# Performance work log

Measured on AMD Instinct MI355X. Metric: run time of the kernel, lower is better.

Reference implementation:

```python
import jax, jax.numpy as jnp
import numpy as np

ALPHA = 0.2  # LeakyReLU negative slope (self.alpha)
NEG_INF = -1e9


def setup_inputs() -> dict:
    key = jax.random.key(0)
    k1, k2, k3, k4, k5 = jax.random.split(key, 5)
    N, Fin, Fout = 8192, 256, 128
    return {
        "input": jax.random.normal(k1, (N, Fin), dtype=jnp.float32),
        "W": jax.random.normal(k2, (Fin, Fout), dtype=jnp.float32) * 0.1,
        "c1": jax.random.normal(k3, (Fout, 1), dtype=jnp.float32) * 0.1,
        "c2": jax.random.normal(k4, (Fout, 1), dtype=jnp.float32) * 0.1,
        "adj": jax.random.randint(k5, (N, N), 0, 2, dtype=jnp.int32),
        "M": N,
    }


def reference(input, W, c1, c2, adj, M):
    # h: [N, Fout]
    h = input @ W
    # valid neighbor j for row x: adj[x, j] > 0 and h[j].sum() != 0
    valid = (adj[:M] > 0) & (jnp.sum(h, axis=1) != 0.0)[None, :]  # [M, N]
    # e[x, j] = leakyrelu(h[x] @ c1 + h[j] @ c2)
    s_dst = (h[:M] @ c1)            # [M, 1]
    s_src = (h @ c2).T              # [1, N]
    e = jax.nn.leaky_relu(s_dst + s_src, negative_slope=ALPHA)
    e = jnp.where(valid, e, NEG_INF)
    attn = jax.nn.softmax(e, axis=1)
    attn = jnp.where(valid, attn, 0.0)  # rows with no neighbors -> all-zero weights
    # dropout is identity at inference (training=False); pool=0 branch skipped
    h_prime = attn @ h              # [M, Fout]
    return jax.nn.elu(h_prime)
```

## Files before the change

kernel.cpp:

```cpp
#include <hip/hip_runtime.h>
#include <math.h>

typedef __attribute__((ext_vector_type(8))) short bf16x8;
typedef __attribute__((ext_vector_type(4))) float f32x4;

#define GAT_ALPHA 0.2f

static __device__ __forceinline__ unsigned short f2bf(float x) {
    unsigned u = __float_as_uint(x);
    u += 0x7fffu + ((u >> 16) & 1u);
    return (unsigned short)(u >> 16);
}
static __device__ __forceinline__ float bf2f(unsigned short b) {
    return __uint_as_float(((unsigned)b) << 16);
}

__global__ __launch_bounds__(512)
void k_prep(const float* __restrict__ input, const float* __restrict__ W,
            const float* __restrict__ c1, const float* __restrict__ c2,
            unsigned short* __restrict__ hb, float* __restrict__ ssx,
            float* __restrict__ sd, int N, int Fin, int Fout)
{
    __shared__ float in_lds[4][256];
    __shared__ float red[4][3];
    const int tid = threadIdx.x;
    const int r0 = blockIdx.x * 4;
    for (int idx = tid; idx < 4 * Fin; idx += 512) {
        int r = idx / Fin, c = idx - r * Fin;
        in_lds[r][c] = input[(size_t)(r0 + r) * Fin + c];
    }
    if (tid < 12) ((float*)red)[tid] = 0.f;
    __syncthreads();
    const int y = tid >> 7, f = tid & 127;
    float acc = 0.f;
    for (int k = 0; k < Fin; ++k)
        acc = fmaf(in_lds[y][k], W[(size_t)k * Fout + f], acc);
    const int row = r0 + y;
    hb[(size_t)row * Fout + f] = f2bf(acc);
    float rs = acc, sv = acc * c2[f], dv = acc * c1[f];
    for (int off = 32; off > 0; off >>= 1) {
        rs += __shfl_xor(rs, off);
        sv += __shfl_xor(sv, off);
        dv += __shfl_xor(dv, off);
    }
    if ((tid & 63) == 0) {
        atomicAdd(&red[y][0], rs);
        atomicAdd(&red[y][1], sv);
        atomicAdd(&red[y][2], dv);
    }
    __syncthreads();
    if (f == 0) {
        float rsum = red[y][0];
        ssx[row] = (rsum != 0.f) ? red[y][1] : -1e30f;
        sd[row]  = red[y][2];
    }
}

__global__ __launch_bounds__(1024)
void k_smax(const float* __restrict__ ssx, float* __restrict__ smax, int N)
{
    __shared__ float red[16];
    const int tid = threadIdx.x;
    float m = -3e38f;
    for (int i = tid; i < N; i += 1024) m = fmaxf(m, ssx[i]);
    for (int off = 32; off > 0; off >>= 1) m = fmaxf(m, __shfl_xor(m, off));
    if ((tid & 63) == 0) red[tid >> 6] = m;
    __syncthreads();
    if (tid == 0) {
        float mm = red[0];
        for (int i = 1; i < 16; ++i) mm = fmaxf(mm, red[i]);
        smax[0] = mm;
    }
}

__global__ __launch_bounds__(256)
void k_transpose(const unsigned short* __restrict__ hb, unsigned short* __restrict__ ht,
                 int N, int Fout)
{
    __shared__ unsigned short t[64][65];
    const int bx = blockIdx.x;
    const int by = blockIdx.y;
    const int tid = threadIdx.x;
    for (int i = 0; i < 16; ++i) {
        int idx = i * 256 + tid; int r = idx >> 6, c = idx & 63;
        t[r][c] = hb[(size_t)(bx * 64 + r) * Fout + by * 64 + c];
    }
    __syncthreads();
    for (int i = 0; i < 16; ++i) {
        int idx = i * 256 + tid; int r = idx >> 6, c = idx & 63;
        ht[(size_t)(by * 64 + r) * N + bx * 64 + c] = t[c][r];
    }
}

__global__ __launch_bounds__(512, 4)
void k_attn(const int* __restrict__ adj, const unsigned short* __restrict__ ht,
            const float* __restrict__ ssx, const float* __restrict__ sd,
            const float* __restrict__ smaxp, unsigned short* __restrict__ part,
            float* __restrict__ dpart, int N, int M, int chunk)
{
    extern __shared__ char smem[];
    unsigned* bits = (unsigned*)smem;
    char* btile = smem + 128 * (chunk >> 3);

    const int tid = threadIdx.x;
    const int rb  = blockIdx.x * 128;
    const int j0  = blockIdx.y * chunk;
    const int wpr = chunk >> 5;
    const int NT  = wpr;

    {
        const int gpr16 = chunk >> 4;
        const int gsh = 31 - __clz(gpr16);
        const int groups = 128 << gsh;
        unsigned short* bsh = (unsigned short*)smem;
        for (int g = tid; g < groups; g += 512) {
            const int rl = g >> gsh;
            const int jg = g & (gpr16 - 1);
            const int* ap = adj + (size_t)(rb + rl) * N + j0 + jg * 16;
            int4 v0 = *(const int4*)ap;
            int4 v1 = *(const int4*)(ap + 4);
            int4 v2 = *(const int4*)(ap + 8);
            int4 v3 = *(const int4*)(ap + 12);
            unsigned b = (unsigned)(v0.x > 0)         | ((unsigned)(v0.y > 0) << 1)
                       | ((unsigned)(v0.z > 0) << 2)  | ((unsigned)(v0.w > 0) << 3)
                       | ((unsigned)(v1.x > 0) << 4)  | ((unsigned)(v1.y > 0) << 5)
                       | ((unsigned)(v1.z > 0) << 6)  | ((unsigned)(v1.w > 0) << 7)
                       | ((unsigned)(v2.x > 0) << 8)  | ((unsigned)(v2.y > 0) << 9)
                       | ((unsigned)(v2.z > 0) << 10) | ((unsigned)(v2.w > 0) << 11)
                       | ((unsigned)(v3.x > 0) << 12) | ((unsigned)(v3.y > 0) << 13)
                       | ((unsigned)(v3.z > 0) << 14) | ((unsigned)(v3.w > 0) << 15);
            bsh[(rl * wpr + ((jg >> 1) ^ (rl & 7))) * 2 + (jg & 1)] = (unsigned short)b;
        }
    }

    const int w  = tid >> 6;
    const int l  = tid & 63;
    const int am = l & 15;
    const int kg = l >> 4;
    const int ams = am & 7;

    const int rl0 = w * 16 + am;
    const int r0 = rb + rl0;
    const float s0 = sd[r0];
    const float sm = smaxp[0];
    const float vb0 = s0 + sm;
    const float m0 = fmaxf(vb0, GAT_ALPHA * vb0);
    const int bw0 = rl0 * wpr;
    const float* __restrict__ sbase = ssx + j0 + 8 * kg;

    const int fw = tid >> 2, jp = tid & 3;
    const unsigned short* __restrict__ gstage = ht + (size_t)fw * N + j0 + jp * 8;
    const int cw = fw >> 4, amw = fw & 15;
    const int wslot = (((cw & 1) << 2) | jp) ^ (amw & 7);
    const int waddr = (fw >> 5) * 2048 + amw * 128 + wslot * 16;

    const int roffE = am * 128 + ((0 | kg) ^ ams) * 16;
    const int roffO = am * 128 + ((4 | kg) ^ ams) * 16;

    f32x4 acc[8];
    #pragma unroll
    for (int c = 0; c < 8; ++c) acc[c] = (f32x4){0.f, 0.f, 0.f, 0.f};
    float d0 = 0.f;

    __syncthreads();

    bf16x8 REG = *(const bf16x8*)gstage;
    float4 sC0 = *(const float4*)(sbase);
    float4 sC1 = *(const float4*)(sbase + 4);
    float4 sN0, sN1;

    auto PBUILD = [&](unsigned bw, const float4& u0, const float4& u1) -> bf16x8 {
        bf16x8 af;
        unsigned short* pu = (unsigned short*)&af;
        const float* f0 = (const float*)&u0;
        const float* f1 = (const float*)&u1;
        float d = 0.f;
        #pragma unroll
        for (int i = 0; i < 4; ++i) {
            float v = s0 + f0[i];
            float e = fminf(fmaxf(v, GAT_ALPHA * v) - m0, 0.f);
            float p = (bw & (1u << i)) ? __expf(e) : 0.f;
            pu[i] = f2bf(p); d += p;
        }
        #pragma unroll
        for (int i = 0; i < 4; ++i) {
            float v = s0 + f1[i];
            float e = fminf(fmaxf(v, GAT_ALPHA * v) - m0, 0.f);
            float p = (bw & (16u << i)) ? __expf(e) : 0.f;
            pu[4 + i] = f2bf(p); d += p;
        }
        d0 += d;
        return af;
    };

    auto STEP = [&](int jt, int par, float4& p0, float4& p1, float4& q0, float4& q1) {
        *(bf16x8*)(btile + par * 8192 + waddr) = REG;
        __syncthreads();
        const char* bt = btile + par * 8192;
        bf16x8 b0 = *(const bf16x8*)(bt + roffE);
        bf16x8 b1 = *(const bf16x8*)(bt + roffO);
        bf16x8 b2 = *(const bf16x8*)(bt + 2048 + roffE);
        bf16x8 b3 = *(const bf16x8*)(bt + 2048 + roffO);
        const unsigned bb = bits[bw0 + (jt ^ ams)] >> (8 * kg);
        const int nj = ((jt + 1 < NT) ? jt + 1 : 0) * 32;
        REG = *(const bf16x8*)(gstage + nj);
        q0 = *(const float4*)(sbase + nj);
        q1 = *(const float4*)(sbase + nj + 4);
        bf16x8 af = PBUILD(bb, p0, p1);
        acc[0] = __builtin_amdgcn_mfma_f32_16x16x32_bf16(af, b0, acc[0], 0, 0, 0);
        acc[1] = __builtin_amdgcn_mfma_f32_16x16x32_bf16(af, b1, acc[1], 0, 0, 0);
        acc[2] = __builtin_amdgcn_mfma_f32_16x16x32_bf16(af, b2, acc[2], 0, 0, 0);
        acc[3] = __builtin_amdgcn_mfma_f32_16x16x32_bf16(af, b3, acc[3], 0, 0, 0);
        bf16x8 b4 = *(const bf16x8*)(bt + 4096 + roffE);
        bf16x8 b5 = *(const bf16x8*)(bt + 4096 + roffO);
        bf16x8 b6 = *(const bf16x8*)(bt + 6144 + roffE);
        bf16x8 b7 = *(const bf16x8*)(bt + 6144 + roffO);
        acc[4] = __builtin_amdgcn_mfma_f32_16x16x32_bf16(af, b4, acc[4], 0, 0, 0);
        acc[5] = __builtin_amdgcn_mfma_f32_16x16x32_bf16(af, b5, acc[5], 0, 0, 0);
        acc[6] = __builtin_amdgcn_mfma_f32_16x16x32_bf16(af, b6, acc[6], 0, 0, 0);
        acc[7] = __builtin_amdgcn_mfma_f32_16x16x32_bf16(af, b7, acc[7], 0, 0, 0);
    };

    for (int jt = 0; jt + 1 < NT; jt += 2) {
        STEP(jt,     0, sC0, sC1, sN0, sN1);
        STEP(jt + 1, 1, sN0, sN1, sC0, sC1);
    }
    if (NT & 1) STEP(NT - 1, 0, sC0, sC1, sN0, sN1);

    d0 += __shfl_xor(d0, 16);
    d0 += __shfl_xor(d0, 32);
    if (kg == 0) dpart[(size_t)blockIdx.y * M + r0] = d0;

    unsigned short* pb = part + (size_t)blockIdx.y * M * 128
                       + ((((size_t)blockIdx.x * 8 + w) * 64 + l) * 32);
    #pragma unroll
    for (int ec = 0; ec < 4; ++ec) {
        const f32x4 x = acc[ec * 2];
        const f32x4 y = acc[ec * 2 + 1];
        bf16x8 pv;
        unsigned short* pp = (unsigned short*)&pv;
        pp[0] = f2bf(x[0]); pp[1] = f2bf(x[1]); pp[2] = f2bf(x[2]); pp[3] = f2bf(x[3]);
        pp[4] = f2bf(y[0]); pp[5] = f2bf(y[1]); pp[6] = f2bf(y[2]); pp[7] = f2bf(y[3]);
        *(bf16x8*)(pb + ec * 8) = pv;
    }
}

__global__ __launch_bounds__(256)
void k_dsum(const float* __restrict__ dpart, float* __restrict__ denom, int M, int NS)
{
    const int r = blockIdx.x * 256 + threadIdx.x;
    if (r < M) {
        float d = 0.f;
        for (int s = 0; s < NS; ++s) d += dpart[(size_t)s * M + r];
        denom[r] = d;
    }
}

__global__ __launch_bounds__(256)
void k_combine(const unsigned short* __restrict__ part, const float* __restrict__ denom,
               float* __restrict__ out, int M, int NS)
{
    const int idx = blockIdx.x * 256 + threadIdx.x;
    const int rbk = idx >> 11;
    const int rem = idx & 2047;
    const int w  = rem >> 8;
    const int l  = (rem >> 2) & 63;
    const int ec = rem & 3;
    const int am = l & 15, kg = l >> 4;

    float sums[8] = {0.f, 0.f, 0.f, 0.f, 0.f, 0.f, 0.f, 0.f};
    const unsigned short* p = part + (size_t)idx * 8;
    for (int s = 0; s < NS; ++s) {
        bf16x8 v = *(const bf16x8*)(p + (size_t)s * M * 128);
        const unsigned short* vp = (const unsigned short*)&v;
        #pragma unroll
        for (int i = 0; i < 8; ++i) sums[i] += bf2f(vp[i]);
    }
    const int rbase = rbk * 128 + w * 16 + kg * 4;
    #pragma unroll
    for (int reg = 0; reg < 4; ++reg) {
        const float dd = denom[rbase + reg];
        const float inv = (dd > 0.f) ? 1.f / dd : 0.f;
        #pragma unroll
        for (int half = 0; half < 2; ++half) {
            float x = sums[half * 4 + reg] * inv;
            x = (x > 0.f) ? x : expm1f(x);
            out[(size_t)(rbase + reg) * 128 + (ec * 2 + half) * 16 + am] = x;
        }
    }
}

extern "C" void kernel_launch(void* const* d_in, const int* in_sizes, int n_in,
                              void* d_out, int out_size, void* d_ws, size_t ws_size,
                              hipStream_t stream)
{
    const float* input = (const float*)d_in[0];
    const float* W     = (const float*)d_in[1];
    const float* c1    = (const float*)d_in[2];
    const float* c2    = (const float*)d_in[3];
    const int*   adj   = (const int*)d_in[4];

    const int Fout = in_sizes[2];
    const int Fin  = in_sizes[1] / Fout;
    const int N    = in_sizes[0] / Fin;
    const int M    = out_size / Fout;
    float* out = (float*)d_out;

    char* ws = (char*)d_ws;
    const size_t o_hb   = 0;
    const size_t o_ht   = o_hb + (size_t)N * Fout * 2;
    const size_t o_ssx  = o_ht + (size_t)N * Fout * 2;
    const size_t o_sd   = o_ssx + (size_t)N * 4;
    const size_t o_smax = o_sd + (size_t)N * 4;
    const size_t o_den  = o_smax + 64;
    const size_t o_dpart = o_den + (((size_t)M * 4 + 63) & ~63ULL);

    int NS = 16;
    size_t o_part = 0;
    while (NS >= 1) {
        size_t op = (o_dpart + (size_t)NS * M * 4 + 15) & ~15ULL;
        if (op + (size_t)NS * M * Fout * 2 <= ws_size) { o_part = op; break; }
        NS >>= 1;
    }
    const int chunk = N / NS;

    unsigned short* hb = (unsigned short*)(ws + o_hb);
    unsigned short* ht = (unsigned short*)(ws + o_ht);
    float* ssx   = (float*)(ws + o_ssx);
    float* sd    = (float*)(ws + o_sd);
    float* smax  = (float*)(ws + o_smax);
    float* denom = (float*)(ws + o_den);
    float* dpart = (float*)(ws + o_dpart);
    unsigned short* part = (unsigned short*)(ws + o_part);

    k_prep<<<N / 4, 512, 0, stream>>>(input, W, c1, c2, hb, ssx, sd, N, Fin, Fout);
    k_smax<<<1, 1024, 0, stream>>>(ssx, smax, N);
    k_transpose<<<dim3(N / 64, Fout / 64), 256, 0, stream>>>(hb, ht, N, Fout);

    const size_t smem_bytes = 128 * (size_t)(chunk >> 3) + 2 * 8192;
    k_attn<<<dim3(M / 128, NS), 512, smem_bytes, stream>>>(
        adj, ht, ssx, sd, smax, part, dpart, N, M, chunk);

    k_dsum<<<(M + 255) / 256, 256, 0, stream>>>(dpart, denom, M, NS);
    k_combine<<<M * Fout / 8 / 256, 256, 0, stream>>>(part, denom, out, M, NS);
}
```

Measured before the change: 160.0 us.

## Restructure attention kernel: direct adj register loads, 256-column LDS tiles, fixed NS=8

The attention kernel no longer packs adjacency into an LDS bitmask up front. Each lane now loads its adj ints directly from global memory, prefetched two k-steps ahead. The h^T tile is staged in 64KB LDS chunks of 256 columns with an XOR swizzle, and ssx values are cached in LDS, giving four barrier phases per block instead of one per 32 columns. The split count is fixed at 8 rather than chosen adaptively from workspace size. This cuts barriers and the bitmask prepass, but the fixed 64KB static LDS limits occupancy and exposes the stage loads without double buffering.

```diff
diff --git a/kernel.cpp b/kernel.cpp
--- a/kernel.cpp
+++ b/kernel.cpp
@@ -5,6 +5,7 @@
 typedef __attribute__((ext_vector_type(4))) float f32x4;
 
 #define GAT_ALPHA 0.2f
+#define NS 8
 
 static __device__ __forceinline__ unsigned short f2bf(float x) {
     unsigned u = __float_as_uint(x);
@@ -96,143 +97,102 @@
 void k_attn(const int* __restrict__ adj, const unsigned short* __restrict__ ht,
             const float* __restrict__ ssx, const float* __restrict__ sd,
             const float* __restrict__ smaxp, unsigned short* __restrict__ part,
-            float* __restrict__ dpart, int N, int M, int chunk)
-{
-    extern __shared__ char smem[];
-    unsigned* bits = (unsigned*)smem;
-    char* btile = smem + 128 * (chunk >> 3);
-
-    const int tid = threadIdx.x;
-    const int rb  = blockIdx.x * 128;
-    const int j0  = blockIdx.y * chunk;
-    const int wpr = chunk >> 5;
-    const int NT  = wpr;
-
-    {
-        const int gpr16 = chunk >> 4;
-        const int gsh = 31 - __clz(gpr16);
-        const int groups = 128 << gsh;
-        unsigned short* bsh = (unsigned short*)smem;
-        for (int g = tid; g < groups; g += 512) {
-            const int rl = g >> gsh;
-            const int jg = g & (gpr16 - 1);
-            const int* ap = adj + (size_t)(rb + rl) * N + j0 + jg * 16;
-            int4 v0 = *(const int4*)ap;
-            int4 v1 = *(const int4*)(ap + 4);
-            int4 v2 = *(const int4*)(ap + 8);
-            int4 v3 = *(const int4*)(ap + 12);
-            unsigned b = (unsigned)(v0.x > 0)         | ((unsigned)(v0.y > 0) << 1)
-                       | ((unsigned)(v0.z > 0) << 2)  | ((unsigned)(v0.w > 0) << 3)
-                       | ((unsigned)(v1.x > 0) << 4)  | ((unsigned)(v1.y > 0) << 5)
-                       | ((unsigned)(v1.z > 0) << 6)  | ((unsigned)(v1.w > 0) << 7)
-                       | ((unsigned)(v2.x > 0) << 8)  | ((unsigned)(v2.y > 0) << 9)
-                       | ((unsigned)(v2.z > 0) << 10) | ((unsigned)(v2.w > 0) << 11)
-                       | ((unsigned)(v3.x > 0) << 12) | ((unsigned)(v3.y > 0) << 13)
-                       | ((unsigned)(v3.z > 0) << 14) | ((unsigned)(v3.w > 0) << 15);
-            bsh[(rl * wpr + ((jg >> 1) ^ (rl & 7))) * 2 + (jg & 1)] = (unsigned short)b;
-        }
-    }
-
-    const int w  = tid >> 6;
-    const int l  = tid & 63;
-    const int am = l & 15;
-    const int kg = l >> 4;
-    const int ams = am & 7;
-
-    const int rl0 = w * 16 + am;
-    const int r0 = rb + rl0;
-    const float s0 = sd[r0];
+            float* __restrict__ dpart, int N, int M)
+{
+    __shared__ char btile[65536];
+    __shared__ float sxl[256];
+
+    const int tid = threadIdx.x;
+    const int w = tid >> 6, l = tid & 63, am = l & 15, kg = l >> 4, ams = am & 7;
+    const int bi = blockIdx.x, bj = blockIdx.y;
+    const int jch = N / NS;
+    const int j0 = bj * jch;
+    const int row = bi * 128 + w * 16 + am;
+
+    const float s0 = sd[row];
     const float sm = smaxp[0];
-    const float vb0 = s0 + sm;
-    const float m0 = fmaxf(vb0, GAT_ALPHA * vb0);
-    const int bw0 = rl0 * wpr;
-    const float* __restrict__ sbase = ssx + j0 + 8 * kg;
-
-    const int fw = tid >> 2, jp = tid & 3;
-    const unsigned short* __restrict__ gstage = ht + (size_t)fw * N + j0 + jp * 8;
-    const int cw = fw >> 4, amw = fw & 15;
-    const int wslot = (((cw & 1) << 2) | jp) ^ (amw & 7);
-    const int waddr = (fw >> 5) * 2048 + amw * 128 + wslot * 16;
-
-    const int roffE = am * 128 + ((0 | kg) ^ ams) * 16;
-    const int roffO = am * 128 + ((4 | kg) ^ ams) * 16;
+    const float vb = s0 + sm;
+    const float m0 = fmaxf(vb, GAT_ALPHA * vb);
+
+    const int fb  = tid >> 5;
+    const int pos = tid & 31;
+    const int rbl = am * 512;
+
+    const int* __restrict__ aptr = adj + (size_t)row * N + j0 + kg * 8;
 
     f32x4 acc[8];
     #pragma unroll
     for (int c = 0; c < 8; ++c) acc[c] = (f32x4){0.f, 0.f, 0.f, 0.f};
     float d0 = 0.f;
 
-    __syncthreads();
-
-    bf16x8 REG = *(const bf16x8*)gstage;
-    float4 sC0 = *(const float4*)(sbase);
-    float4 sC1 = *(const float4*)(sbase + 4);
-    float4 sN0, sN1;
-
-    auto PBUILD = [&](unsigned bw, const float4& u0, const float4& u1) -> bf16x8 {
+    int4 cA0 = *(const int4*)(aptr);
+    int4 cA1 = *(const int4*)(aptr + 4);
+    int4 cB0 = *(const int4*)(aptr + 32);
+    int4 cB1 = *(const int4*)(aptr + 36);
+
+    auto KS = [&](int q, int4& c0, int4& c1) {
+        const int ks = q & 7;
+        float4 x0 = *(const float4*)&sxl[ks * 32 + kg * 8];
+        float4 x1 = *(const float4*)&sxl[ks * 32 + kg * 8 + 4];
         bf16x8 af;
-        unsigned short* pu = (unsigned short*)&af;
-        const float* f0 = (const float*)&u0;
-        const float* f1 = (const float*)&u1;
-        float d = 0.f;
-        #pragma unroll
-        for (int i = 0; i < 4; ++i) {
-            float v = s0 + f0[i];
-            float e = fminf(fmaxf(v, GAT_ALPHA * v) - m0, 0.f);
-            float p = (bw & (1u << i)) ? __expf(e) : 0.f;
-            pu[i] = f2bf(p); d += p;
-        }
-        #pragma unroll
-        for (int i = 0; i < 4; ++i) {
-            float v = s0 + f1[i];
-            float e = fminf(fmaxf(v, GAT_ALPHA * v) - m0, 0.f);
-            float p = (bw & (16u << i)) ? __expf(e) : 0.f;
-            pu[4 + i] = f2bf(p); d += p;
-        }
-        d0 += d;
-        return af;
+        {
+            unsigned short* pu = (unsigned short*)&af;
+            const int* ai0 = (const int*)&c0;
+            const int* ai1 = (const int*)&c1;
+            const float* f0 = (const float*)&x0;
+            const float* f1 = (const float*)&x1;
+            float d = 0.f;
+            #pragma unroll
+            for (int i = 0; i < 4; ++i) {
+                float v = s0 + f0[i];
+                float e = fminf(fmaxf(v, GAT_ALPHA * v) - m0, 0.f);
+                float p = (ai0[i] > 0) ? __expf(e) : 0.f;
+                pu[i] = f2bf(p); d += p;
+            }
+            #pragma unroll
+            for (int i = 0; i < 4; ++i) {
+                float v = s0 + f1[i];
+                float e = fminf(fmaxf(v, GAT_ALPHA * v) - m0, 0.f);
+                float p = (ai1[i] > 0) ? __expf(e) : 0.f;
+                pu[4 + i] = f2bf(p); d += p;
+            }
+            d0 += d;
+        }
+        const int qq = (q + 2 < 4 * 8) ? q + 2 : 4 * 8 - 1;
+        c0 = *(const int4*)(aptr + qq * 32);
+        c1 = *(const int4*)(aptr + qq * 32 + 4);
+        const int sb = rbl + (((ks * 4 + kg) ^ ams) << 4);
+        #pragma unroll
+        for (int c = 0; c < 8; ++c) {
+            bf16x8 bf = *(const bf16x8*)(btile + sb + c * 8192);
+            acc[c] = __builtin_amdgcn_mfma_f32_16x16x32_bf16(af, bf, acc[c], 0, 0, 0);
+        }
     };
 
-    auto STEP = [&](int jt, int par, float4& p0, float4& p1, float4& q0, float4& q1) {
-        *(bf16x8*)(btile + par * 8192 + waddr) = REG;
+    for (int ch = 0; ch < 4; ++ch) {
+        if (ch) __syncthreads();
+        #pragma unroll
+        for (int it = 0; it < 8; ++it) {
+            const int f = it * 16 + fb;
+            bf16x8 v = *(const bf16x8*)(ht + (size_t)f * N + j0 + ch * 256 + pos * 8);
+            *(bf16x8*)(btile + f * 512 + ((pos ^ (f & 7)) << 4)) = v;
+        }
+        if (tid < 64)
+            *(float4*)&sxl[tid * 4] = *(const float4*)(ssx + j0 + ch * 256 + tid * 4);
         __syncthreads();
-        const char* bt = btile + par * 8192;
-        bf16x8 b0 = *(const bf16x8*)(bt + roffE);
-        bf16x8 b1 = *(const bf16x8*)(bt + roffO);
-        bf16x8 b2 = *(const bf16x8*)(bt + 2048 + roffE);
-        bf16x8 b3 = *(const bf16x8*)(bt + 2048 + roffO);
-        const unsigned bb = bits[bw0 + (jt ^ ams)] >> (8 * kg);
-        const int nj = ((jt + 1 < NT) ? jt + 1 : 0) * 32;
-        REG = *(const bf16x8*)(gstage + nj);
-        q0 = *(const float4*)(sbase + nj);
-        q1 = *(const float4*)(sbase + nj + 4);
-        bf16x8 af = PBUILD(bb, p0, p1);
-        acc[0] = __builtin_amdgcn_mfma_f32_16x16x32_bf16(af, b0, acc[0], 0, 0, 0);
-        acc[1] = __builtin_amdgcn_mfma_f32_16x16x32_bf16(af, b1, acc[1], 0, 0, 0);
-        acc[2] = __builtin_amdgcn_mfma_f32_16x16x32_bf16(af, b2, acc[2], 0, 0, 0);
-        acc[3] = __builtin_amdgcn_mfma_f32_16x16x32_bf16(af, b3, acc[3], 0, 0, 0);
-        bf16x8 b4 = *(const bf16x8*)(bt + 4096 + roffE);
-        bf16x8 b5 = *(const bf16x8*)(bt + 4096 + roffO);
-        bf16x8 b6 = *(const bf16x8*)(bt + 6144 + roffE);
-        bf16x8 b7 = *(const bf16x8*)(bt + 6144 + roffO);
-        acc[4] = __builtin_amdgcn_mfma_f32_16x16x32_bf16(af, b4, acc[4], 0, 0, 0);
-        acc[5] = __builtin_amdgcn_mfma_f32_16x16x32_bf16(af, b5, acc[5], 0, 0, 0);
-        acc[6] = __builtin_amdgcn_mfma_f32_16x16x32_bf16(af, b6, acc[6], 0, 0, 0);
-        acc[7] = __builtin_amdgcn_mfma_f32_16x16x32_bf16(af, b7, acc[7], 0, 0, 0);
-    };
-
-    for (int jt = 0; jt + 1 < NT; jt += 2) {
-        STEP(jt,     0, sC0, sC1, sN0, sN1);
-        STEP(jt + 1, 1, sN0, sN1, sC0, sC1);
-    }
-    if (NT & 1) STEP(NT - 1, 0, sC0, sC1, sN0, sN1);
+        #pragma unroll
+        for (int ks = 0; ks < 8; ks += 2) {
+            KS(ch * 8 + ks,     cA0, cA1);
+            KS(ch * 8 + ks + 1, cB0, cB1);
+        }
+    }
 
     d0 += __shfl_xor(d0, 16);
     d0 += __shfl_xor(d0, 32);
-    if (kg == 0) dpart[(size_t)blockIdx.y * M + r0] = d0;
-
-    unsigned short* pb = part + (size_t)blockIdx.y * M * 128
-                       + ((((size_t)blockIdx.x * 8 + w) * 64 + l) * 32);
+    if (kg == 0) dpart[(size_t)bj * M + row] = d0;
+
+    unsigned short* pb = part + (size_t)bj * M * 128
+                       + ((((size_t)bi * 8 + w) * 64 + l) * 32);
     #pragma unroll
     for (int ec = 0; ec < 4; ++ec) {
         const f32x4 x = acc[ec * 2];
@@ -246,19 +206,19 @@
 }
 
 __global__ __launch_bounds__(256)
-void k_dsum(const float* __restrict__ dpart, float* __restrict__ denom, int M, int NS)
+void k_dsum(const float* __restrict__ dpart, float* __restrict__ denom, int M, int nsp)
 {
     const int r = blockIdx.x * 256 + threadIdx.x;
     if (r < M) {
         float d = 0.f;
-        for (int s = 0; s < NS; ++s) d += dpart[(size_t)s * M + r];
+        for (int s = 0; s < nsp; ++s) d += dpart[(size_t)s * M + r];
         denom[r] = d;
     }
 }
 
 __global__ __launch_bounds__(256)
 void k_combine(const unsigned short* __restrict__ part, const float* __restrict__ denom,
-               float* __restrict__ out, int M, int NS)
+               float* __restrict__ out, int M, int nsp)
 {
     const int idx = blockIdx.x * 256 + threadIdx.x;
     const int rbk = idx >> 11;
@@ -270,7 +230,7 @@
 
     float sums[8] = {0.f, 0.f, 0.f, 0.f, 0.f, 0.f, 0.f, 0.f};
     const unsigned short* p = part + (size_t)idx * 8;
-    for (int s = 0; s < NS; ++s) {
+    for (int s = 0; s < nsp; ++s) {
         bf16x8 v = *(const bf16x8*)(p + (size_t)s * M * 128);
         const unsigned short* vp = (const unsigned short*)&v;
         #pragma unroll
@@ -314,15 +274,7 @@
     const size_t o_smax = o_sd + (size_t)N * 4;
     const size_t o_den  = o_smax + 64;
     const size_t o_dpart = o_den + (((size_t)M * 4 + 63) & ~63ULL);
-
-    int NS = 16;
-    size_t o_part = 0;
-    while (NS >= 1) {
-        size_t op = (o_dpart + (size_t)NS * M * 4 + 15) & ~15ULL;
-        if (op + (size_t)NS * M * Fout * 2 <= ws_size) { o_part = op; break; }
-        NS >>= 1;
-    }
-    const int chunk = N / NS;
+    const size_t o_part = (o_dpart + (size_t)NS * M * 4 + 63) & ~63ULL;
 
     unsigned short* hb = (unsigned short*)(ws + o_hb);
     unsigned short* ht = (unsigned short*)(ws + o_ht);
@@ -337,9 +289,8 @@
     k_smax<<<1, 1024, 0, stream>>>(ssx, smax, N);
     k_transpose<<<dim3(N / 64, Fout / 64), 256, 0, stream>>>(hb, ht, N, Fout);
 
-    const size_t smem_bytes = 128 * (size_t)(chunk >> 3) + 2 * 8192;
-    k_attn<<<dim3(M / 128, NS), 512, smem_bytes, stream>>>(
-        adj, ht, ssx, sd, smax, part, dpart, N, M, chunk);
+    k_attn<<<dim3(M / 128, NS), 512, 0, stream>>>(
+        adj, ht, ssx, sd, smax, part, dpart, N, M);
 
     k_dsum<<<(M + 255) / 256, 256, 0, stream>>>(dpart, denom, M, NS);
     k_combine<<<M * Fout / 8 / 256, 256, 0, stream>>>(part, denom, out, M, NS);
```

Result: faster. 150.0 us (-6.2%).
